# Optimization experiments

Measured on AMD Instinct MI355X. Metric: run time of the kernel, lower is better.

The kernel has to match this reference:

```python
import jax, jax.numpy as jnp
import numpy as np

NEG_SLOPE = 0.2
EPS = 1e-16


def _glorot(key, shape):
    fan_in, fan_out = shape[0], shape[-1]
    lim = jnp.sqrt(6.0 / (fan_in + fan_out))
    return jax.random.uniform(key, shape, jnp.float32, -lim, lim)


def setup_inputs() -> dict:
    key = jax.random.key(0)
    ks = jax.random.split(key, 20)
    N, E = 10000, 160000
    dims = [(256, 1024), (1024, 1024), (1024, 512), (512, 128)]
    inp = {
        "x": jax.random.normal(ks[0], (N, 256), jnp.float32),
        "edge_index": jax.random.randint(ks[1], (2, E), 0, N, jnp.int64),
    }
    ki = 2
    for li, (din, dout) in enumerate(dims, start=1):
        inp[f"W{li}"] = _glorot(ks[ki], (din, dout)); ki += 1
        inp[f"as{li}"] = _glorot(ks[ki], (1, dout))[0]; ki += 1
        inp[f"ad{li}"] = _glorot(ks[ki], (1, dout))[0]; ki += 1
        inp[f"b{li}"] = jnp.zeros((dout,), jnp.float32)
    return inp


def gat_conv(x, src, dst, W, a_src, a_dst, b, N):
    # x: [N, din]; src/dst: [E'] (self-loops already appended)
    h = x @ W                                   # [N, dout]
    s_src = h @ a_src                           # [N] per-node source score
    s_dst = h @ a_dst                           # [N] per-node target score
    e = s_src[src] + s_dst[dst]                 # [E'] attention logits
    e = jnp.where(e > 0, e, NEG_SLOPE * e)      # LeakyReLU(0.2)
    # segment softmax over incoming edges of each target node
    m = jax.ops.segment_max(e, dst, num_segments=N)
    ex = jnp.exp(e - m[dst])
    denom = jax.ops.segment_sum(ex, dst, num_segments=N)
    alpha = ex / (denom[dst] + EPS)             # [E']
    # scatter-aggregate weighted messages
    msg = alpha[:, None] * h[src]               # [E', dout]
    out = jax.ops.segment_sum(msg, dst, num_segments=N)
    return out + b


def reference(x, edge_index, W1, as1, ad1, b1, W2, as2, ad2, b2,
              W3, as3, ad3, b3, W4, as4, ad4, b4):
    N = x.shape[0]
    loops = jnp.arange(N, dtype=edge_index.dtype)
    src = jnp.concatenate([edge_index[0], loops])
    dst = jnp.concatenate([edge_index[1], loops])
    h = gat_conv(x, src, dst, W1, as1, ad1, b1, N)
    h = jax.nn.relu(h)  # dropout is identity in eval mode
    h = gat_conv(h, src, dst, W2, as2, ad2, b2, N)
    h = jax.nn.relu(h)
    h = gat_conv(h, src, dst, W3, as3, ad3, b3, N)
    h = jax.nn.relu(h)
    h = gat_conv(h, src, dst, W4, as4, ad4, b4, N)
    return jax.nn.log_softmax(h, axis=1)
```

## Files before the change

kernel.cpp:

```cpp
#include <hip/hip_runtime.h>
#include <math.h>

#define NEG_SLOPE 0.2f
#define EPS_F 1e-16f
typedef long long ll;

typedef __attribute__((ext_vector_type(4))) float f32x4;
typedef __attribute__((ext_vector_type(8))) short bf16x8;

__device__ __forceinline__ unsigned short bf16_of(float f) {
  unsigned u = __float_as_uint(f);
  u += 0x7fffu + ((u >> 16) & 1u);
  return (unsigned short)(u >> 16);
}
__device__ __forceinline__ float bf16_back(unsigned short s) {
  return __uint_as_float((unsigned)s << 16);
}

__device__ __forceinline__ void gload16(const void* g, void* l) {
  __builtin_amdgcn_global_load_lds((const __attribute__((address_space(1))) void*)g,
                                   (__attribute__((address_space(3))) void*)l, 16, 0, 0);
}

__global__ void detect_int64_kernel(const unsigned int* __restrict__ w, int E,
                                    int* __restrict__ flag) {
  __shared__ int nz;
  if (threadIdx.x == 0) nz = 0;
  __syncthreads();
  int cnt = E < 2048 ? E : 2048;
  int local = 0;
  for (int i = threadIdx.x; i < cnt; i += blockDim.x)
    if (w[2 * i + 1] != 0u) local++;
  if (local) atomicAdd(&nz, local);
  __syncthreads();
  if (threadIdx.x == 0) *flag = (nz == 0) ? 1 : 0;
}

__device__ __forceinline__ void edge_at(const int* __restrict__ ew, int E, int e,
                                        int is64, int& s, int& d) {
  if (is64) { s = ew[2 * e]; d = ew[2 * E + 2 * e]; }
  else      { s = ew[e];     d = ew[E + e]; }
}

__global__ void count_deg_kernel(const int* __restrict__ ew, int E, int* deg,
                                 const int* __restrict__ flag) {
  int is64 = *flag;
  int e = blockIdx.x * blockDim.x + threadIdx.x;
  if (e < E) {
    int s, d;
    edge_at(ew, E, e, is64, s, d);
    atomicAdd(&deg[d], 1);
  }
}

__global__ void scan_kernel(const int* __restrict__ deg, int* rowptr, int* cursor, int N) {
  __shared__ int sums[1024];
  int tid = threadIdx.x;
  int chunk = (N + 1023) >> 10;
  int start = tid * chunk;
  int end = start + chunk; if (end > N) end = N;
  int s = 0;
  for (int i = start; i < end; ++i) s += deg[i] + 1;
  sums[tid] = s;
  __syncthreads();
  for (int off = 1; off < 1024; off <<= 1) {
    int v = (tid >= off) ? sums[tid - off] : 0;
    __syncthreads();
    sums[tid] += v;
    __syncthreads();
  }
  int run = (tid == 0) ? 0 : sums[tid - 1];
  for (int i = start; i < end; ++i) {
    rowptr[i] = run; cursor[i] = run;
    run += deg[i] + 1;
  }
  if (tid == 1023) rowptr[N] = sums[1023];
}

__global__ void fill_kernel(const int* __restrict__ ew, int E, int N, int* cursor,
                            int* csr, const int* __restrict__ flag) {
  int is64 = *flag;
  int i = blockIdx.x * blockDim.x + threadIdx.x;
  if (i < E) {
    int s, d;
    edge_at(ew, E, i, is64, s, d);
    int pos = atomicAdd(&cursor[d], 1);
    csr[pos] = s;
  } else if (i < E + N) {
    int n = i - E;
    int pos = atomicAdd(&cursor[n], 1);
    csr[pos] = n;
  }
}

__global__ __launch_bounds__(256) void convert_w_all_kernel(
    const float* __restrict__ W0, const float* __restrict__ W1,
    const float* __restrict__ W2, const float* __restrict__ W3,
    short* __restrict__ B0, short* __restrict__ B1,
    short* __restrict__ B2, short* __restrict__ B3) {
  const int Ks[4]  = {256, 1024, 1024, 512};
  const int Ncs[4] = {1024, 1024, 512, 128};
  int z = blockIdx.z;
  int K = Ks[z], Nc = Ncs[z];
  int k0 = blockIdx.x * 32, n0 = blockIdx.y * 32;
  if (k0 >= K || n0 >= Nc) return;
  const float* W = z == 0 ? W0 : (z == 1 ? W1 : (z == 2 ? W2 : W3));
  short* Bt = z == 0 ? B0 : (z == 1 ? B1 : (z == 2 ? B2 : B3));
  __shared__ float t[32][33];
  int r = threadIdx.x >> 3;
  int c4 = (threadIdx.x & 7) * 4;
  float4 v = *(const float4*)&W[(ll)(k0 + r) * Nc + n0 + c4];
  t[r][c4] = v.x; t[r][c4 + 1] = v.y; t[r][c4 + 2] = v.z; t[r][c4 + 3] = v.w;
  __syncthreads();
  float f0 = t[c4 + 0][r], f1 = t[c4 + 1][r], f2 = t[c4 + 2][r], f3 = t[c4 + 3][r];
  short4 hp = make_short4((short)bf16_of(f0), (short)bf16_of(f1),
                          (short)bf16_of(f2), (short)bf16_of(f3));
  *(short4*)&Bt[(ll)(n0 + r) * K + k0 + c4] = hp;
}

__global__ void wvec_kernel(const float* __restrict__ W, const float* __restrict__ as,
                            const float* __restrict__ ad, float* __restrict__ ws,
                            float* __restrict__ wd, int K, int Nc) {
  int wid = threadIdx.x >> 6, lane = threadIdx.x & 63;
  int k = blockIdx.x * 4 + wid;
  if (k >= K) return;
  const float* row = W + (ll)k * Nc;
  float a = 0.f, b = 0.f;
  for (int j = lane; j < Nc; j += 64) {
    float w = row[j];
    a += w * as[j];
    b += w * ad[j];
  }
#pragma unroll
  for (int o = 32; o > 0; o >>= 1) {
    a += __shfl_xor(a, o, 64);
    b += __shfl_xor(b, o, 64);
  }
  if (lane == 0) { ws[k] = a; wd[k] = b; }
}

__global__ void score_gemv_kernel(const float* __restrict__ x, const float* __restrict__ ws,
                                  const float* __restrict__ wd, float* __restrict__ s_src,
                                  float* __restrict__ s_dst, int N) {
  int wid = threadIdx.x >> 6, lane = threadIdx.x & 63;
  int n = blockIdx.x * 4 + wid;
  if (n >= N) return;
  float4 xv = *(const float4*)&x[(ll)n * 256 + lane * 4];
  float4 wsv = *(const float4*)&ws[lane * 4];
  float4 wdv = *(const float4*)&wd[lane * 4];
  float a = xv.x * wsv.x + xv.y * wsv.y + xv.z * wsv.z + xv.w * wsv.w;
  float b = xv.x * wdv.x + xv.y * wdv.y + xv.z * wdv.z + xv.w * wdv.w;
#pragma unroll
  for (int o = 32; o > 0; o >>= 1) {
    a += __shfl_xor(a, o, 64);
    b += __shfl_xor(b, o, 64);
  }
  if (lane == 0) { s_src[n] = a; s_dst[n] = b; }
}

__global__ __launch_bounds__(256) void agg_x_kernel(
    const float* __restrict__ x, const float* __restrict__ ssrc,
    const float* __restrict__ sdst, const int* __restrict__ rowptr,
    const int* __restrict__ csr, short* __restrict__ outH, int N) {
  int wid = threadIdx.x >> 6, lane = threadIdx.x & 63;
  int node = blockIdx.x * 4 + wid;
  if (node >= N) return;
  int rs = rowptr[node];
  int nd = rowptr[node + 1] - rs;
  float sd = sdst[node];
  int d0 = lane * 4;

  float a0 = 0.f, a1 = 0.f, a2 = 0.f, a3 = 0.f;
  auto accum = [&](int s, float w) {
    float4 xv = *(const float4*)&x[(ll)s * 256 + d0];
    a0 += w * xv.x; a1 += w * xv.y; a2 += w * xv.z; a3 += w * xv.w;
  };

  if (nd <= 64) {
    int srcl = 0;
    float e = -1e30f;
    if (lane < nd) {
      srcl = csr[rs + lane];
      float t = ssrc[srcl] + sd;
      e = t > 0.f ? t : NEG_SLOPE * t;
    }
    float m = e;
#pragma unroll
    for (int o = 32; o > 0; o >>= 1) m = fmaxf(m, __shfl_xor(m, o, 64));
    float ex = (lane < nd) ? __expf(e - m) : 0.f;
    float den = ex;
#pragma unroll
    for (int o = 32; o > 0; o >>= 1) den += __shfl_xor(den, o, 64);
    float al = ex / (den + EPS_F);
    int i = 0;
    for (; i + 4 <= nd; i += 4) {
      int s0 = __shfl(srcl, i, 64), s1 = __shfl(srcl, i + 1, 64);
      int s2 = __shfl(srcl, i + 2, 64), s3 = __shfl(srcl, i + 3, 64);
      float w0 = __shfl(al, i, 64), w1 = __shfl(al, i + 1, 64);
      float w2 = __shfl(al, i + 2, 64), w3 = __shfl(al, i + 3, 64);
      accum(s0, w0); accum(s1, w1); accum(s2, w2); accum(s3, w3);
    }
    for (; i < nd; ++i) accum(__shfl(srcl, i, 64), __shfl(al, i, 64));
  } else {
    float m = -1e30f;
    for (int i = lane; i < nd; i += 64) {
      float t = ssrc[csr[rs + i]] + sd;
      t = t > 0.f ? t : NEG_SLOPE * t;
      m = fmaxf(m, t);
    }
#pragma unroll
    for (int o = 32; o > 0; o >>= 1) m = fmaxf(m, __shfl_xor(m, o, 64));
    float den = 0.f;
    for (int i = lane; i < nd; i += 64) {
      float t = ssrc[csr[rs + i]] + sd;
      t = t > 0.f ? t : NEG_SLOPE * t;
      den += __expf(t - m);
    }
#pragma unroll
    for (int o = 32; o > 0; o >>= 1) den += __shfl_xor(den, o, 64);
    float inv = 1.f / (den + EPS_F);
    for (int i = 0; i < nd; ++i) {
      int s = csr[rs + i];
      float t = ssrc[s] + sd;
      t = t > 0.f ? t : NEG_SLOPE * t;
      accum(s, __expf(t - m) * inv);
    }
  }

  unsigned short h0 = bf16_of(a0), h1 = bf16_of(a1), h2 = bf16_of(a2), h3 = bf16_of(a3);
  short4 hp = make_short4((short)h0, (short)h1, (short)h2, (short)h3);
  short4 lp = make_short4((short)bf16_of(a0 - bf16_back(h0)),
                          (short)bf16_of(a1 - bf16_back(h1)),
                          (short)bf16_of(a2 - bf16_back(h2)),
                          (short)bf16_of(a3 - bf16_back(h3)));
  ll base = (ll)node * 512 + d0;
  *(short4*)&outH[base] = hp;
  *(short4*)&outH[base + 256] = lp;
}

template <int HBF16, int SPLIT, int BIASRELU, int SCORES>
__global__ __launch_bounds__(256) void gemm_mfma_kernel(
    const short* __restrict__ A, const short* __restrict__ Bt,
    void* __restrict__ Cv, const float* __restrict__ a_src,
    const float* __restrict__ a_dst, const float* __restrict__ bias,
    float* __restrict__ partS, float* __restrict__ partD, int M, int Nc, int K) {
  __shared__ char Ah[SPLIT ? 8192 : 4096];
  __shared__ char Bs[8192];
  char* Al = Ah + 4096;
  int tid = threadIdx.x;

  int nwg = gridDim.x * gridDim.y;
  int hb = blockIdx.y * gridDim.x + blockIdx.x;
  int xcd = hb & 7, q = nwg >> 3, r = nwg & 7;
  int lg = (xcd < r ? xcd * (q + 1) : r * (q + 1) + (xcd - r) * q) + (hb >> 3);
  int bx = lg % gridDim.x, by = lg / gridDim.x;
  int bm = by * 64, bn = bx * 128;

  int lane = tid & 63, wid = tid >> 6;
  int wr = wid >> 1, wc = wid & 1;
  int AS = SPLIT ? 2 * K : K;

  f32x4 acc[2][4];
#pragma unroll
  for (int m = 0; m < 2; ++m)
#pragma unroll
    for (int n = 0; n < 4; ++n) acc[m][n] = (f32x4){0.f, 0.f, 0.f, 0.f};

  int srow = tid >> 2;
  int cphys = tid & 3;
  int swz = (srow >> 1) & 3;
  int clog = (cphys ^ swz) * 8;
  int ra = bm + srow; if (ra > M - 1) ra = M - 1;
  const short* aP0 = A + (ll)ra * AS + clog;
  const short* bP0 = Bt + (ll)(bn + srow) * K + clog;
  const short* bP1 = Bt + (ll)(bn + srow + 64) * K + clog;
  int dstOff = tid * 16;

  int lrow = lane & 15;
  int lchunk = ((lane >> 4) ^ ((lrow >> 1) & 3)) * 16;
  int fOffA = (wr * 32 + lrow) * 64 + lchunk;
  int fOffB = (wc * 64 + lrow) * 64 + lchunk;

  for (int kt = 0; kt < K; kt += 32) {
    gload16(aP0 + kt, Ah + dstOff);
    if constexpr (SPLIT) gload16(aP0 + K + kt, Al + dstOff);
    gload16(bP0 + kt, Bs + dstOff);
    gload16(bP1 + kt, Bs + 4096 + dstOff);
    __syncthreads();
    bf16x8 ah[2], al[2], bfr[4];
#pragma unroll
    for (int m = 0; m < 2; ++m) {
      ah[m] = *(const bf16x8*)(Ah + fOffA + m * 1024);
      if constexpr (SPLIT) al[m] = *(const bf16x8*)(Al + fOffA + m * 1024);
    }
#pragma unroll
    for (int n = 0; n < 4; ++n) bfr[n] = *(const bf16x8*)(Bs + fOffB + n * 1024);
#pragma unroll
    for (int m = 0; m < 2; ++m)
#pragma unroll
      for (int n = 0; n < 4; ++n) {
        acc[m][n] = __builtin_amdgcn_mfma_f32_16x16x32_bf16(ah[m], bfr[n], acc[m][n], 0, 0, 0);
        if constexpr (SPLIT)
          acc[m][n] = __builtin_amdgcn_mfma_f32_16x16x32_bf16(al[m], bfr[n], acc[m][n], 0, 0, 0);
      }
    __syncthreads();
  }

  int crow0 = bm + wr * 32 + (lane >> 4) * 4;
  int ccol0 = bn + wc * 64 + (lane & 15);
  float bv4[4];
  if constexpr (BIASRELU) {
#pragma unroll
    for (int n = 0; n < 4; ++n) bv4[n] = bias[ccol0 + n * 16];
  }
#pragma unroll
  for (int m = 0; m < 2; ++m) {
#pragma unroll
    for (int j = 0; j < 4; ++j) {
      int row = crow0 + m * 16 + j;
      if (row < M) {
#pragma unroll
        for (int n = 0; n < 4; ++n) {
          float v = acc[m][n][j];
          if constexpr (BIASRELU) v = fmaxf(v + bv4[n], 0.f);
          if (HBF16) ((unsigned short*)Cv)[(ll)row * Nc + ccol0 + n * 16] = bf16_of(v);
          else       ((float*)Cv)[(ll)row * Nc + ccol0 + n * 16] = v;
        }
      }
    }
  }

  if constexpr (SCORES) {
    float as4[4], ad4[4];
#pragma unroll
    for (int n = 0; n < 4; ++n) {
      as4[n] = a_src[ccol0 + n * 16];
      ad4[n] = a_dst[ccol0 + n * 16];
    }
    int p = bx * 2 + wc;
#pragma unroll
    for (int m = 0; m < 2; ++m) {
#pragma unroll
      for (int j = 0; j < 4; ++j) {
        float ps = acc[m][0][j] * as4[0] + acc[m][1][j] * as4[1] +
                   acc[m][2][j] * as4[2] + acc[m][3][j] * as4[3];
        float pd = acc[m][0][j] * ad4[0] + acc[m][1][j] * ad4[1] +
                   acc[m][2][j] * ad4[2] + acc[m][3][j] * ad4[3];
#pragma unroll
        for (int o = 1; o < 16; o <<= 1) {
          ps += __shfl_xor(ps, o, 64);
          pd += __shfl_xor(pd, o, 64);
        }
        int row = crow0 + m * 16 + j;
        if ((lane & 15) == 0 && row < M) {
          partS[(ll)p * M + row] = ps;
          partD[(ll)p * M + row] = pd;
        }
      }
    }
  }
}

__global__ void score_reduce_kernel(const float* __restrict__ partS,
                                    const float* __restrict__ partD,
                                    float* __restrict__ s_src, float* __restrict__ s_dst,
                                    int N, int NP) {
  int i = blockIdx.x * blockDim.x + threadIdx.x;
  if (i >= N) return;
  float a = 0.f, b = 0.f;
  for (int p = 0; p < NP; ++p) {
    a += partS[(ll)p * N + i];
    b += partD[(ll)p * N + i];
  }
  s_src[i] = a;
  s_dst[i] = b;
}

template <int DOUT, int HIN_BF16, int OUTB16, int LOGSM>
__global__ __launch_bounds__(256) void agg_wave_kernel(
    const void* __restrict__ hv, const float* __restrict__ ssrc,
    const float* __restrict__ sdst, const int* __restrict__ rowptr,
    const int* __restrict__ csr, const float* __restrict__ bias,
    float* __restrict__ outF, short* __restrict__ outH, int N) {
  constexpr int NH = (DOUT >= 512) ? DOUT / 512 : 1;
  constexpr int DPL = (DOUT >= 512) ? 8 : DOUT / 64;
  int wid = threadIdx.x >> 6, lane = threadIdx.x & 63;
  int node = blockIdx.x * 4 + wid;
  if (node >= N) return;
  int rs = rowptr[node];
  int nd = rowptr[node + 1] - rs;
  float sd = sdst[node];
  int d0 = lane * DPL;

  float acc[NH][DPL];
#pragma unroll
  for (int hh = 0; hh < NH; ++hh)
#pragma unroll
    for (int k = 0; k < DPL; ++k) acc[hh][k] = 0.f;

  auto accum = [&](int s, float w) {
    if constexpr (HIN_BF16) {
      const unsigned short* hp = (const unsigned short*)hv + (ll)s * DOUT + d0;
#pragma unroll
      for (int hh = 0; hh < NH; ++hh) {
        bf16x8 qv = *(const bf16x8*)(hp + hh * 512);
#pragma unroll
        for (int k = 0; k < 8; ++k)
          acc[hh][k] += w * bf16_back((unsigned short)qv[k]);
      }
    } else {
      const float* hp = (const float*)hv + (ll)s * DOUT + d0;
#pragma unroll
      for (int k = 0; k < DPL; ++k) acc[0][k] += w * hp[k];
    }
  };

  if (nd <= 64) {
    int srcl = 0;
    float e = -1e30f;
    if (lane < nd) {
      srcl = csr[rs + lane];
      float t = ssrc[srcl] + sd;
      e = t > 0.f ? t : NEG_SLOPE * t;
    }
    float m = e;
#pragma unroll
    for (int o = 32; o > 0; o >>= 1) m = fmaxf(m, __shfl_xor(m, o, 64));
    float ex = (lane < nd) ? __expf(e - m) : 0.f;
    float den = ex;
#pragma unroll
    for (int o = 32; o > 0; o >>= 1) den += __shfl_xor(den, o, 64);
    float al = ex / (den + EPS_F);

    int i = 0;
    for (; i + 4 <= nd; i += 4) {
      int s0 = __shfl(srcl, i, 64), s1 = __shfl(srcl, i + 1, 64);
      int s2 = __shfl(srcl, i + 2, 64), s3 = __shfl(srcl, i + 3, 64);
      float w0 = __shfl(al, i, 64), w1 = __shfl(al, i + 1, 64);
      float w2 = __shfl(al, i + 2, 64), w3 = __shfl(al, i + 3, 64);
      accum(s0, w0); accum(s1, w1); accum(s2, w2); accum(s3, w3);
    }
    for (; i < nd; ++i) accum(__shfl(srcl, i, 64), __shfl(al, i, 64));
  } else {
    float m = -1e30f;
    for (int i = lane; i < nd; i += 64) {
      float t = ssrc[csr[rs + i]] + sd;
      t = t > 0.f ? t : NEG_SLOPE * t;
      m = fmaxf(m, t);
    }
#pragma unroll
    for (int o = 32; o > 0; o >>= 1) m = fmaxf(m, __shfl_xor(m, o, 64));
    float den = 0.f;
    for (int i = lane; i < nd; i += 64) {
      float t = ssrc[csr[rs + i]] + sd;
      t = t > 0.f ? t : NEG_SLOPE * t;
      den += __expf(t - m);
    }
#pragma unroll
    for (int o = 32; o > 0; o >>= 1) den += __shfl_xor(den, o, 64);
    float inv = 1.f / (den + EPS_F);
    for (int i = 0; i < nd; ++i) {
      int s = csr[rs + i];
      float t = ssrc[s] + sd;
      t = t > 0.f ? t : NEG_SLOPE * t;
      accum(s, __expf(t - m) * inv);
    }
  }

  if constexpr (OUTB16) {
#pragma unroll
    for (int hh = 0; hh < NH; ++hh) {
      int d = hh * 512 + d0;
      bf16x8 hp8;
#pragma unroll
      for (int k = 0; k < 8; ++k) {
        float v = fmaxf(acc[hh][k] + bias[d + k], 0.f);
        hp8[k] = (short)bf16_of(v);
      }
      *(bf16x8*)&outH[(ll)node * DOUT + d] = hp8;
    }
  } else if constexpr (LOGSM) {
    float v0 = acc[0][0] + bias[d0 + 0];
    float v1 = acc[0][1] + bias[d0 + 1];
    float mx = fmaxf(v0, v1);
#pragma unroll
    for (int o = 32; o > 0; o >>= 1) mx = fmaxf(mx, __shfl_xor(mx, o, 64));
    float s = __expf(v0 - mx) + __expf(v1 - mx);
#pragma unroll
    for (int o = 32; o > 0; o >>= 1) s += __shfl_xor(s, o, 64);
    float ls = logf(s);
    outF[(ll)node * DOUT + d0 + 0] = v0 - mx - ls;
    outF[(ll)node * DOUT + d0 + 1] = v1 - mx - ls;
  } else {
#pragma unroll
    for (int k = 0; k < DPL; ++k)
      outF[(ll)node * DOUT + d0 + k] = acc[0][k] + bias[d0 + k];
  }
}

extern "C" void kernel_launch(void* const* d_in, const int* in_sizes, int n_in,
                              void* d_out, int out_size, void* d_ws, size_t ws_size,
                              hipStream_t stream) {
  const float* x = (const float*)d_in[0];
  const int* ew = (const int*)d_in[1];
  int N = in_sizes[0] / 256;
  int E = in_sizes[1] / 2;

  const float* W[4]   = {(const float*)d_in[2],  (const float*)d_in[6],
                         (const float*)d_in[10], (const float*)d_in[14]};
  const float* Asv[4] = {(const float*)d_in[3],  (const float*)d_in[7],
                         (const float*)d_in[11], (const float*)d_in[15]};
  const float* Adv[4] = {(const float*)d_in[4],  (const float*)d_in[8],
                         (const float*)d_in[12], (const float*)d_in[16]};
  const float* Bv[4]  = {(const float*)d_in[5],  (const float*)d_in[9],
                         (const float*)d_in[13], (const float*)d_in[17]};
  const int din[4]  = {256, 1024, 1024, 512};
  const int dout[4] = {1024, 1024, 512, 128};

  char* ws = (char*)d_ws;
  size_t off = 0;
  auto alloc = [&](size_t bytes) {
    void* p = ws + off;
    off += (bytes + 255) & ~(size_t)255;
    return p;
  };
  unsigned short* hB = (unsigned short*)alloc((size_t)N * 1024 * 2);
  float* hF   = (float*)alloc((size_t)N * 128 * 4);
  short* bufP = (short*)alloc((size_t)N * 512 * 2);
  short* bufQ = (short*)alloc((size_t)N * 1024 * 2);
  short* bufR = (short*)alloc((size_t)N * 1024 * 2);
  float* s_src = (float*)alloc((size_t)N * 4);
  float* s_dst = (float*)alloc((size_t)N * 4);
  float* partS = (float*)alloc((size_t)16 * N * 4);
  float* partD = (float*)alloc((size_t)16 * N * 4);
  float* wvS  = (float*)alloc((size_t)256 * 4);
  float* wvD  = (float*)alloc((size_t)256 * 4);
  int* deg    = (int*)alloc((size_t)(N + 1) * 4);
  int* rowptr = (int*)alloc((size_t)(N + 1) * 4);
  int* cursor = (int*)alloc((size_t)(N + 1) * 4);
  int* csr    = (int*)alloc((size_t)(E + N) * 4);
  int* flag   = (int*)alloc(256);
  short* Bt[4];
  for (int l = 0; l < 4; ++l) Bt[l] = (short*)alloc((size_t)dout[l] * din[l] * 2);

  detect_int64_kernel<<<1, 256, 0, stream>>>((const unsigned int*)ew, E, flag);
  hipMemsetAsync(deg, 0, (size_t)(N + 1) * 4, stream);
  count_deg_kernel<<<(E + 255) / 256, 256, 0, stream>>>(ew, E, deg, flag);
  scan_kernel<<<1, 1024, 0, stream>>>(deg, rowptr, cursor, N);
  fill_kernel<<<(E + N + 255) / 256, 256, 0, stream>>>(ew, E, N, cursor, csr, flag);

  {
    dim3 cg(32, 32, 4);
    convert_w_all_kernel<<<cg, 256, 0, stream>>>(W[0], W[1], W[2], W[3],
                                                 Bt[0], Bt[1], Bt[2], Bt[3]);
  }
  wvec_kernel<<<64, 256, 0, stream>>>(W[0], Asv[0], Adv[0], wvS, wvD, 256, 1024);

  int ngrp = (N + 3) / 4;
  int mgrp = (N + 63) / 64;
  {
    score_gemv_kernel<<<ngrp, 256, 0, stream>>>(x, wvS, wvD, s_src, s_dst, N);
    agg_x_kernel<<<ngrp, 256, 0, stream>>>(x, s_src, s_dst, rowptr, csr, bufP, N);
    dim3 gg(dout[0] / 128, mgrp);
    gemm_mfma_kernel<1, 1, 1, 0><<<gg, 256, 0, stream>>>(
        bufP, Bt[0], bufQ, nullptr, nullptr, Bv[0], partS, partD, N, dout[0], din[0]);
  }
  {
    dim3 gg(dout[1] / 128, mgrp);
    gemm_mfma_kernel<1, 0, 0, 1><<<gg, 256, 0, stream>>>(
        bufQ, Bt[1], hB, Asv[1], Adv[1], nullptr, partS, partD, N, dout[1], din[1]);
    score_reduce_kernel<<<(N + 255) / 256, 256, 0, stream>>>(partS, partD, s_src, s_dst,
                                                             N, (dout[1] / 128) * 2);
    agg_wave_kernel<1024, 1, 1, 0><<<ngrp, 256, 0, stream>>>(
        hB, s_src, s_dst, rowptr, csr, Bv[1], nullptr, bufR, N);
  }
  {
    dim3 gg(dout[2] / 128, mgrp);
    gemm_mfma_kernel<1, 0, 0, 1><<<gg, 256, 0, stream>>>(
        bufR, Bt[2], hB, Asv[2], Adv[2], nullptr, partS, partD, N, dout[2], din[2]);
    score_reduce_kernel<<<(N + 255) / 256, 256, 0, stream>>>(partS, partD, s_src, s_dst,
                                                             N, (dout[2] / 128) * 2);
    agg_wave_kernel<512, 1, 1, 0><<<ngrp, 256, 0, stream>>>(
        hB, s_src, s_dst, rowptr, csr, Bv[2], nullptr, bufQ, N);
  }
  {
    dim3 gg(dout[3] / 128, mgrp);
    gemm_mfma_kernel<0, 0, 0, 1><<<gg, 256, 0, stream>>>(
        bufQ, Bt[3], hF, Asv[3], Adv[3], nullptr, partS, partD, N, dout[3], din[3]);
    score_reduce_kernel<<<(N + 255) / 256, 256, 0, stream>>>(partS, partD, s_src, s_dst,
                                                             N, (dout[3] / 128) * 2);
    agg_wave_kernel<128, 0, 0, 1><<<ngrp, 256, 0, stream>>>(
        hF, s_src, s_dst, rowptr, csr, Bv[3], (float*)d_out, nullptr, N);
  }
}
```

Before: 273.5 us.

## Compute next-layer attention scores in aggregation epilogue via precomputed W·a vectors

Precomputes W·a_src and W·a_dst for layers 1, 3 and 4 in one batched kernel. The aggregation epilogues of layers 2 and 3 then dot their post-ReLU output with the next layer's vectors, giving the next layer's node scores directly. This drops the score epilogue and partial buffers from the layer 3 and 4 GEMMs and removes two score_reduce launches. The edge-gather loop is also unrolled from 4 to 8. Scores now come from the fp32 activations before bf16 rounding, so they differ slightly from scores computed off the rounded GEMM output.

```diff
diff --git a/kernel.cpp b/kernel.cpp
--- a/kernel.cpp
+++ b/kernel.cpp
@@ -118,12 +118,22 @@
   *(short4*)&Bt[(ll)(n0 + r) * K + k0 + c4] = hp;
 }
 
-__global__ void wvec_kernel(const float* __restrict__ W, const float* __restrict__ as,
-                            const float* __restrict__ ad, float* __restrict__ ws,
-                            float* __restrict__ wd, int K, int Nc) {
+__global__ void wvec_all_kernel(
+    const float* __restrict__ W0, const float* __restrict__ as0, const float* __restrict__ ad0,
+    const float* __restrict__ W2, const float* __restrict__ as2, const float* __restrict__ ad2,
+    const float* __restrict__ W3, const float* __restrict__ as3, const float* __restrict__ ad3,
+    float* __restrict__ wvS, float* __restrict__ wvD) {
+  const int Ks[3]   = {256, 1024, 512};
+  const int Ncs[3]  = {1024, 512, 128};
+  const int offs[3] = {0, 256, 1280};
+  int zi = blockIdx.y;
+  int K = Ks[zi], Nc = Ncs[zi];
   int wid = threadIdx.x >> 6, lane = threadIdx.x & 63;
   int k = blockIdx.x * 4 + wid;
   if (k >= K) return;
+  const float* W  = zi == 0 ? W0 : (zi == 1 ? W2 : W3);
+  const float* as = zi == 0 ? as0 : (zi == 1 ? as2 : as3);
+  const float* ad = zi == 0 ? ad0 : (zi == 1 ? ad2 : ad3);
   const float* row = W + (ll)k * Nc;
   float a = 0.f, b = 0.f;
   for (int j = lane; j < Nc; j += 64) {
@@ -136,7 +146,7 @@
     a += __shfl_xor(a, o, 64);
     b += __shfl_xor(b, o, 64);
   }
-  if (lane == 0) { ws[k] = a; wd[k] = b; }
+  if (lane == 0) { wvS[offs[zi] + k] = a; wvD[offs[zi] + k] = b; }
 }
 
 __global__ void score_gemv_kernel(const float* __restrict__ x, const float* __restrict__ ws,
@@ -193,12 +203,15 @@
     for (int o = 32; o > 0; o >>= 1) den += __shfl_xor(den, o, 64);
     float al = ex / (den + EPS_F);
     int i = 0;
-    for (; i + 4 <= nd; i += 4) {
-      int s0 = __shfl(srcl, i, 64), s1 = __shfl(srcl, i + 1, 64);
-      int s2 = __shfl(srcl, i + 2, 64), s3 = __shfl(srcl, i + 3, 64);
-      float w0 = __shfl(al, i, 64), w1 = __shfl(al, i + 1, 64);
-      float w2 = __shfl(al, i + 2, 64), w3 = __shfl(al, i + 3, 64);
-      accum(s0, w0); accum(s1, w1); accum(s2, w2); accum(s3, w3);
+    for (; i + 8 <= nd; i += 8) {
+      int ssx[8]; float ww[8];
+#pragma unroll
+      for (int u = 0; u < 8; ++u) {
+        ssx[u] = __shfl(srcl, i + u, 64);
+        ww[u] = __shfl(al, i + u, 64);
+      }
+#pragma unroll
+      for (int u = 0; u < 8; ++u) accum(ssx[u], ww[u]);
     }
     for (; i < nd; ++i) accum(__shfl(srcl, i, 64), __shfl(al, i, 64));
   } else {
@@ -376,12 +389,14 @@
   s_dst[i] = b;
 }
 
-template <int DOUT, int HIN_BF16, int OUTB16, int LOGSM>
+template <int DOUT, int HIN_BF16, int OUTB16, int LOGSM, int SCORENEXT>
 __global__ __launch_bounds__(256) void agg_wave_kernel(
     const void* __restrict__ hv, const float* __restrict__ ssrc,
     const float* __restrict__ sdst, const int* __restrict__ rowptr,
     const int* __restrict__ csr, const float* __restrict__ bias,
-    float* __restrict__ outF, short* __restrict__ outH, int N) {
+    float* __restrict__ outF, short* __restrict__ outH,
+    const float* __restrict__ wvnS, const float* __restrict__ wvnD,
+    float* __restrict__ oSs, float* __restrict__ oSd, int N) {
   constexpr int NH = (DOUT >= 512) ? DOUT / 512 : 1;
   constexpr int DPL = (DOUT >= 512) ? 8 : DOUT / 64;
   int wid = threadIdx.x >> 6, lane = threadIdx.x & 63;
@@ -433,12 +448,15 @@
     float al = ex / (den + EPS_F);
 
     int i = 0;
-    for (; i + 4 <= nd; i += 4) {
-      int s0 = __shfl(srcl, i, 64), s1 = __shfl(srcl, i + 1, 64);
-      int s2 = __shfl(srcl, i + 2, 64), s3 = __shfl(srcl, i + 3, 64);
-      float w0 = __shfl(al, i, 64), w1 = __shfl(al, i + 1, 64);
-      float w2 = __shfl(al, i + 2, 64), w3 = __shfl(al, i + 3, 64);
-      accum(s0, w0); accum(s1, w1); accum(s2, w2); accum(s3, w3);
+    for (; i + 8 <= nd; i += 8) {
+      int ssx[8]; float ww[8];
+#pragma unroll
+      for (int u = 0; u < 8; ++u) {
+        ssx[u] = __shfl(srcl, i + u, 64);
+        ww[u] = __shfl(al, i + u, 64);
+      }
+#pragma unroll
+      for (int u = 0; u < 8; ++u) accum(ssx[u], ww[u]);
     }
     for (; i < nd; ++i) accum(__shfl(srcl, i, 64), __shfl(al, i, 64));
   } else {
@@ -468,6 +486,7 @@
   }
 
   if constexpr (OUTB16) {
+    float ps = 0.f, pd = 0.f;
 #pragma unroll
     for (int hh = 0; hh < NH; ++hh) {
       int d = hh * 512 + d0;
@@ -476,8 +495,20 @@
       for (int k = 0; k < 8; ++k) {
         float v = fmaxf(acc[hh][k] + bias[d + k], 0.f);
         hp8[k] = (short)bf16_of(v);
+        if constexpr (SCORENEXT) {
+          ps += v * wvnS[d + k];
+          pd += v * wvnD[d + k];
+        }
       }
       *(bf16x8*)&outH[(ll)node * DOUT + d] = hp8;
+    }
+    if constexpr (SCORENEXT) {
+#pragma unroll
+      for (int o = 32; o > 0; o >>= 1) {
+        ps += __shfl_xor(ps, o, 64);
+        pd += __shfl_xor(pd, o, 64);
+      }
+      if (lane == 0) { oSs[node] = ps; oSd[node] = pd; }
     }
   } else if constexpr (LOGSM) {
     float v0 = acc[0][0] + bias[d0 + 0];
@@ -529,12 +560,14 @@
   short* bufP = (short*)alloc((size_t)N * 512 * 2);
   short* bufQ = (short*)alloc((size_t)N * 1024 * 2);
   short* bufR = (short*)alloc((size_t)N * 1024 * 2);
-  float* s_src = (float*)alloc((size_t)N * 4);
-  float* s_dst = (float*)alloc((size_t)N * 4);
+  float* s_src  = (float*)alloc((size_t)N * 4);
+  float* s_dst  = (float*)alloc((size_t)N * 4);
+  float* s_src2 = (float*)alloc((size_t)N * 4);
+  float* s_dst2 = (float*)alloc((size_t)N * 4);
   float* partS = (float*)alloc((size_t)16 * N * 4);
   float* partD = (float*)alloc((size_t)16 * N * 4);
-  float* wvS  = (float*)alloc((size_t)256 * 4);
-  float* wvD  = (float*)alloc((size_t)256 * 4);
+  float* wvS  = (float*)alloc((size_t)2048 * 4);
+  float* wvD  = (float*)alloc((size_t)2048 * 4);
   int* deg    = (int*)alloc((size_t)(N + 1) * 4);
   int* rowptr = (int*)alloc((size_t)(N + 1) * 4);
   int* cursor = (int*)alloc((size_t)(N + 1) * 4);
@@ -554,7 +587,12 @@
     convert_w_all_kernel<<<cg, 256, 0, stream>>>(W[0], W[1], W[2], W[3],
                                                  Bt[0], Bt[1], Bt[2], Bt[3]);
   }
-  wvec_kernel<<<64, 256, 0, stream>>>(W[0], Asv[0], Adv[0], wvS, wvD, 256, 1024);
+  {
+    dim3 wg(256, 3);
+    wvec_all_kernel<<<wg, 256, 0, stream>>>(W[0], Asv[0], Adv[0],
+                                            W[2], Asv[2], Adv[2],
+                                            W[3], Asv[3], Adv[3], wvS, wvD);
+  }
 
   int ngrp = (N + 3) / 4;
   int mgrp = (N + 63) / 64;
@@ -563,7 +601,7 @@
     agg_x_kernel<<<ngrp, 256, 0, stream>>>(x, s_src, s_dst, rowptr, csr, bufP, N);
     dim3 gg(dout[0] / 128, mgrp);
     gemm_mfma_kernel<1, 1, 1, 0><<<gg, 256, 0, stream>>>(
-        bufP, Bt[0], bufQ, nullptr, nullptr, Bv[0], partS, partD, N, dout[0], din[0]);
+        bufP, Bt[0], bufQ, nullptr, nullptr, Bv[0], nullptr, nullptr, N, dout[0], din[0]);
   }
   {
     dim3 gg(dout[1] / 128, mgrp);
@@ -571,25 +609,24 @@
         bufQ, Bt[1], hB, Asv[1], Adv[1], nullptr, partS, partD, N, dout[1], din[1]);
     score_reduce_kernel<<<(N + 255) / 256, 256, 0, stream>>>(partS, partD, s_src, s_dst,
                                                              N, (dout[1] / 128) * 2);
-    agg_wave_kernel<1024, 1, 1, 0><<<ngrp, 256, 0, stream>>>(
-        hB, s_src, s_dst, rowptr, csr, Bv[1], nullptr, bufR, N);
+    agg_wave_kernel<1024, 1, 1, 0, 1><<<ngrp, 256, 0, stream>>>(
+        hB, s_src, s_dst, rowptr, csr, Bv[1], nullptr, bufR,
+        wvS + 256, wvD + 256, s_src2, s_dst2, N);
   }
   {
     dim3 gg(dout[2] / 128, mgrp);
-    gemm_mfma_kernel<1, 0, 0, 1><<<gg, 256, 0, stream>>>(
-        bufR, Bt[2], hB, Asv[2], Adv[2], nullptr, partS, partD, N, dout[2], din[2]);
-    score_reduce_kernel<<<(N + 255) / 256, 256, 0, stream>>>(partS, partD, s_src, s_dst,
-                                                             N, (dout[2] / 128) * 2);
-    agg_wave_kernel<512, 1, 1, 0><<<ngrp, 256, 0, stream>>>(
-        hB, s_src, s_dst, rowptr, csr, Bv[2], nullptr, bufQ, N);
+    gemm_mfma_kernel<1, 0, 0, 0><<<gg, 256, 0, stream>>>(
+        bufR, Bt[2], hB, nullptr, nullptr, nullptr, nullptr, nullptr, N, dout[2], din[2]);
+    agg_wave_kernel<512, 1, 1, 0, 1><<<ngrp, 256, 0, stream>>>(
+        hB, s_src2, s_dst2, rowptr, csr, Bv[2], nullptr, bufQ,
+        wvS + 1280, wvD + 1280, s_src, s_dst, N);
   }
   {
     dim3 gg(dout[3] / 128, mgrp);
-    gemm_mfma_kernel<0, 0, 0, 1><<<gg, 256, 0, stream>>>(
-        bufQ, Bt[3], hF, Asv[3], Adv[3], nullptr, partS, partD, N, dout[3], din[3]);
-    score_reduce_kernel<<<(N + 255) / 256, 256, 0, stream>>>(partS, partD, s_src, s_dst,
-                                                             N, (dout[3] / 128) * 2);
-    agg_wave_kernel<128, 0, 0, 1><<<ngrp, 256, 0, stream>>>(
-        hF, s_src, s_dst, rowptr, csr, Bv[3], (float*)d_out, nullptr, N);
-  }
-}
+    gemm_mfma_kernel<0, 0, 0, 0><<<gg, 256, 0, stream>>>(
+        bufQ, Bt[3], hF, nullptr, nullptr, nullptr, nullptr, nullptr, N, dout[3], din[3]);
+    agg_wave_kernel<128, 0, 0, 1, 0><<<ngrp, 256, 0, stream>>>(
+        hF, s_src, s_dst, rowptr, csr, Bv[3], (float*)d_out, nullptr,
+        nullptr, nullptr, nullptr, nullptr, N);
+  }
+}
```

Measured after the change: 271.3 us. About the same (-0.8%).
